# Kernel optimization log

Hardware: AMD Instinct MI355X
Metric: run time of the kernel (lower is better)

## Reference

```python
import jax, jax.numpy as jnp
import numpy as np

B, S, D, H, DFF = 2, 2048, 1024, 16, 4096
DK = D // H
EPS = float(np.finfo(np.float32).eps)  # torch RMSNorm default eps = finfo eps


def rmsnorm(x, g):
    var = jnp.mean(x * x, axis=-1, keepdims=True)
    return x * jax.lax.rsqrt(var + EPS) * g


def rope_cos_sin(seq_len, dim, base=10000.0):
    inv_freq = 1.0 / (base ** (jnp.arange(0, dim, 2, dtype=jnp.float32) / dim))
    t = jnp.arange(seq_len, dtype=jnp.float32)
    freqs = jnp.outer(t, inv_freq)            # [S, dim/2]
    emb = jnp.concatenate([freqs, freqs], -1)  # [S, dim]
    return jnp.cos(emb), jnp.sin(emb)


def rotate_half(x):
    x1, x2 = x[..., : x.shape[-1] // 2], x[..., x.shape[-1] // 2:]
    return jnp.concatenate([-x2, x1], axis=-1)


def setup_inputs() -> dict:
    key = jax.random.key(0)
    ks = jax.random.split(key, 16)
    sc = 0.02
    return {
        "x": jax.random.normal(ks[0], (B, S, D), jnp.float32),
        "wq": jax.random.normal(ks[1], (D, D), jnp.float32) * sc,
        "bq": jnp.zeros((D,), jnp.float32),
        "wk": jax.random.normal(ks[2], (D, D), jnp.float32) * sc,
        "bk": jnp.zeros((D,), jnp.float32),
        "wv": jax.random.normal(ks[3], (D, D), jnp.float32) * sc,
        "bv": jnp.zeros((D,), jnp.float32),
        "wo": jax.random.normal(ks[4], (D, D), jnp.float32) * sc,
        "bo": jnp.zeros((D,), jnp.float32),
        "w1": jax.random.normal(ks[5], (D, DFF), jnp.float32) * sc,
        "b1": jnp.zeros((DFF,), jnp.float32),
        "w2": jax.random.normal(ks[6], (DFF, D), jnp.float32) * sc,
        "b2": jnp.zeros((D,), jnp.float32),
        "g1": jnp.ones((D,), jnp.float32),
        "g2": jnp.ones((D,), jnp.float32),
    }


def reference(x, wq, bq, wk, bk, wv, bv, wo, bo, w1, b1, w2, b2, g1, g2):
    b, s, d = x.shape
    # --- self-attention sublayer (pre-RMSNorm residual) ---
    h = rmsnorm(x, g1)
    q = (h @ wq + bq).reshape(b, s, H, DK).transpose(0, 2, 1, 3)  # [B,H,S,dk]
    k = (h @ wk + bk).reshape(b, s, H, DK).transpose(0, 2, 1, 3)
    v = (h @ wv + bv).reshape(b, s, H, DK).transpose(0, 2, 1, 3)
    cos, sin = rope_cos_sin(s, DK)
    cos = cos[None, None]  # [1,1,S,dk]
    sin = sin[None, None]
    q = q * cos + rotate_half(q) * sin
    k = k * cos + rotate_half(k) * sin
    scores = jnp.einsum("bhqd,bhkd->bhqk", q, k) / jnp.sqrt(jnp.float32(DK))
    p = jax.nn.softmax(scores, axis=-1)
    o = jnp.einsum("bhqk,bhkd->bhqd", p, v)
    o = o.transpose(0, 2, 1, 3).reshape(b, s, d)
    attn_out = o @ wo + bo
    x = x + attn_out
    # --- feed-forward sublayer ---
    h2 = rmsnorm(x, g2)
    ff = jax.nn.relu(h2 @ w1 + b1) @ w2 + b2
    return x + ff
```

## Files before the change

### kernel.cpp

```cpp
#include <hip/hip_runtime.h>
#include <math.h>

typedef unsigned short u16;
typedef __attribute__((ext_vector_type(8))) short bf16x8;
typedef __attribute__((ext_vector_type(4))) float f32x4;
typedef __attribute__((ext_vector_type(4))) unsigned int u32x4;

#define B_ 2
#define S_ 2048
#define D_ 1024
#define H_ 16
#define DK_ 64
#define DFF_ 4096
#define EPS_ 1.1920928955078125e-07f
#define EXP2SC 0.18033688011112042f

__device__ __forceinline__ float bf2f(u16 u) {
  unsigned int v = ((unsigned int)u) << 16;
  return __builtin_bit_cast(float, v);
}
__device__ __forceinline__ u16 f2bf(float f) {
  unsigned int x = __builtin_bit_cast(unsigned int, f);
  x += 0x7fffu + ((x >> 16) & 1u);
  return (u16)(x >> 16);
}

typedef __attribute__((address_space(3))) unsigned int lds_uint;
typedef const __attribute__((address_space(1))) unsigned int glb_uint;
__device__ __forceinline__ void gload16(const void* g, void* l) {
  __builtin_amdgcn_global_load_lds((glb_uint*)g, (lds_uint*)l, 16, 0, 0);
}

__device__ __forceinline__ unsigned int cvtpk(float lo, float hi) {
  unsigned int d;
  asm("v_cvt_pk_bf16_f32 %0, %1, %2" : "=v"(d) : "v"(lo), "v"(hi));
  return d;
}
__device__ __forceinline__ void plswap32(unsigned int& a, unsigned int& b) {
  asm("v_permlane32_swap_b32 %0, %1" : "+v"(a), "+v"(b));
}
__device__ __forceinline__ void plswap16(unsigned int& a, unsigned int& b) {
  asm("v_permlane16_swap_b32 %0, %1" : "+v"(a), "+v"(b));
}

__global__ __launch_bounds__(256) void rope_table(float* __restrict__ cosT,
                                                  float* __restrict__ sinT) {
  int idx = blockIdx.x * 256 + threadIdx.x;
  if (idx >= S_ * 32) return;
  int s = idx >> 5, i = idx & 31;
  double inv = exp(((double)(-2 * i) / (double)DK_) * log(10000.0));
  double ang = (double)s * inv;
  cosT[idx] = (float)cos(ang);
  sinT[idx] = (float)sin(ang);
}

__global__ __launch_bounds__(256) void convertT(const float* __restrict__ src,
                                                u16* __restrict__ dst, int R, int C) {
  __shared__ float t[32][33];
  int c0 = blockIdx.x * 32, r0 = blockIdx.y * 32;
  int tx = threadIdx.x, ty = threadIdx.y;
#pragma unroll
  for (int i = 0; i < 32; i += 8)
    t[ty + i][tx] = src[(size_t)(r0 + ty + i) * C + (c0 + tx)];
  __syncthreads();
#pragma unroll
  for (int i = 0; i < 32; i += 8)
    dst[(size_t)(c0 + ty + i) * R + (r0 + tx)] = f2bf(t[tx][ty + i]);
}

__global__ __launch_bounds__(256) void rmsnorm_k(const float* __restrict__ X,
                                                 const float* __restrict__ g,
                                                 u16* __restrict__ out) {
  const int row = blockIdx.x;
  const float* xr = X + (size_t)row * D_;
  u16* orow = out + (size_t)row * D_;
  const int tid = threadIdx.x;
  float vals[4];
  float s = 0.f;
#pragma unroll
  for (int j = 0; j < 4; j++) {
    float v = xr[tid + j * 256];
    vals[j] = v;
    s += v * v;
  }
#pragma unroll
  for (int off = 32; off > 0; off >>= 1) s += __shfl_down(s, off, 64);
  __shared__ float red[4];
  __shared__ float ssc;
  int lane = tid & 63, wave = tid >> 6;
  if (lane == 0) red[wave] = s;
  __syncthreads();
  if (tid == 0) ssc = 1.0f / sqrtf((red[0] + red[1] + red[2] + red[3]) * (1.0f / D_) + EPS_);
  __syncthreads();
  float sc = ssc;
#pragma unroll
  for (int j = 0; j < 4; j++) {
    int i = tid + j * 256;
    orow[i] = f2bf(vals[j] * sc * g[i]);
  }
}

#define GEMM_KLOOP(APTR, BPTR, KLEN, KLD)                                              \
  for (int k0 = 0; k0 < (KLEN); k0 += 64) {                                            \
    _Pragma("unroll")                                                                  \
    for (int p = 0; p < 2; p++) {                                                      \
      _Pragma("unroll")                                                                \
      for (int c = wave; c < BM / 16; c += 4) {                                        \
        const u16* gp = (APTR) + (size_t)(m0 + c * 16 + lrow) * (KLD) + k0 + p * 32 + lcol; \
        gload16(gp, (char*)As + __builtin_amdgcn_readfirstlane(p * (BM * 64) + c * 1024)); \
      }                                                                                \
      _Pragma("unroll")                                                                \
      for (int c = wave; c < BN / 16; c += 4) {                                        \
        const u16* gp = (BPTR) + (size_t)(n0 + c * 16 + lrow) * (KLD) + k0 + p * 32 + lcol; \
        gload16(gp, (char*)Bs + __builtin_amdgcn_readfirstlane(p * (BN * 64) + c * 1024)); \
      }                                                                                \
    }                                                                                  \
    __syncthreads();                                                                   \
    _Pragma("unroll")                                                                  \
    for (int p = 0; p < 2; p++) {                                                      \
      bf16x8 af[WR], bfv[WC];                                                          \
      _Pragma("unroll")                                                                \
      for (int i = 0; i < WR; i++)                                                     \
        af[i] = *(const bf16x8*)&As[p * (BM * 32) + (wm + i * 16 + l16) * 32 + quad * 8]; \
      _Pragma("unroll")                                                                \
      for (int j = 0; j < WC; j++)                                                     \
        bfv[j] = *(const bf16x8*)&Bs[p * (BN * 32) + (wn + j * 16 + l16) * 32 + quad * 8]; \
      _Pragma("unroll")                                                                \
      for (int i = 0; i < WR; i++)                                                     \
        _Pragma("unroll")                                                              \
        for (int j = 0; j < WC; j++)                                                   \
          acc[i][j] = __builtin_amdgcn_mfma_f32_16x16x32_bf16(af[i], bfv[j], acc[i][j], 0, 0, 0); \
    }                                                                                  \
    __syncthreads();                                                                   \
  }

template <int MODE, int WR, int WC>
__global__ __launch_bounds__(256) void gemm_bt(
    const u16* __restrict__ A, const u16* __restrict__ Bt, const float* __restrict__ bias,
    u16* __restrict__ outB, float* __restrict__ outF, const float* __restrict__ resF,
    int M, int N, int K) {
  constexpr int BM = 2 * WR * 16;
  constexpr int BN = 2 * WC * 16;
  __shared__ u16 As[BM * 64];
  __shared__ u16 Bs[BN * 64];
  const int tid = threadIdx.x;
  const int wave = tid >> 6, lane = tid & 63, quad = lane >> 4, l16 = lane & 15;
  const int wm = (wave >> 1) * (WR * 16), wn = (wave & 1) * (WC * 16);
  const int m0 = blockIdx.y * BM, n0 = blockIdx.x * BN;
  const int lrow = lane >> 2, lcol = (lane & 3) * 8;
  f32x4 acc[WR][WC] = {};
  GEMM_KLOOP(A, Bt, K, K)
#pragma unroll
  for (int i = 0; i < WR; i++)
#pragma unroll
    for (int j = 0; j < WC; j++) {
      int col = n0 + wn + j * 16 + l16;
      float bv = bias[col];
#pragma unroll
      for (int r = 0; r < 4; r++) {
        int row = m0 + wm + i * 16 + quad * 4 + r;
        size_t off = (size_t)row * N + col;
        float v = acc[i][j][r] + bv;
        if constexpr (MODE == 1) v = fmaxf(v, 0.f);
        if constexpr (MODE == 2) outF[off] = v + resF[off];
        else outB[off] = f2bf(v);
      }
    }
}

__global__ __launch_bounds__(256) void gemm_qkv(
    const u16* __restrict__ A, const u16* __restrict__ Bt,
    const float* __restrict__ bq, const float* __restrict__ bk, const float* __restrict__ bv,
    const float* __restrict__ cosT, const float* __restrict__ sinT,
    u16* __restrict__ Qb, u16* __restrict__ Kb, u16* __restrict__ VT, int M, int K) {
  constexpr int WR = 4, WC = 4;
  constexpr int BM = 128, BN = 128;
  __shared__ u16 As[BM * 64];
  __shared__ u16 Bs[BN * 64];
  const int tid = threadIdx.x;
  const int wave = tid >> 6, lane = tid & 63, quad = lane >> 4, l16 = lane & 15;
  const int wm = (wave >> 1) * 64, wn = (wave & 1) * 64;
  const int m0 = blockIdx.y * BM, n0 = blockIdx.x * BN;
  const int lrow = lane >> 2, lcol = (lane & 3) * 8;
  f32x4 acc[WR][WC] = {};
  GEMM_KLOOP(A, Bt, K, K)
  const int g = n0 >> 10;
  if (g < 2) {
    u16* dst = (g == 0) ? Qb : Kb;
    const float* bias = (g == 0) ? bq : bk;
#pragma unroll
    for (int i = 0; i < WR; i++)
#pragma unroll
      for (int jp = 0; jp < 2; jp++) {
        int col0 = n0 + wn + jp * 16 + l16;
        int c0 = col0 & 1023;
        float bv0 = bias[c0], bv1 = bias[c0 + 32];
        int irot = jp * 16 + l16;
        int row0 = m0 + wm + i * 16 + quad * 4;
#pragma unroll
        for (int r = 0; r < 4; r++) {
          int row = row0 + r;
          int s2 = row & 2047;
          float cs = cosT[s2 * 32 + irot];
          float sn = sinT[s2 * 32 + irot];
          float x0 = acc[i][jp][r] + bv0;
          float x1 = acc[i][jp + 2][r] + bv1;
          dst[(size_t)row * D_ + c0]      = f2bf(x0 * cs - x1 * sn);
          dst[(size_t)row * D_ + c0 + 32] = f2bf(x1 * cs + x0 * sn);
        }
      }
  } else {
#pragma unroll
    for (int i = 0; i < WR; i++)
#pragma unroll
      for (int j = 0; j < WC; j++) {
        int col = n0 + wn + j * 16 + l16;
        int c = col & 1023;
        float bvv = bv[c];
        int row0 = m0 + wm + i * 16 + quad * 4;
        int hh = c >> 6, dk = c & 63;
        int b = row0 >> 11, s2 = row0 & 2047;
        ushort4 pv;
        pv.x = f2bf(acc[i][j][0] + bvv);
        pv.y = f2bf(acc[i][j][1] + bvv);
        pv.z = f2bf(acc[i][j][2] + bvv);
        pv.w = f2bf(acc[i][j][3] + bvv);
        *(ushort4*)&VT[(((size_t)(b * H_ + hh)) * DK_ + dk) * S_ + s2] = pv;
      }
  }
}

template <int WR, int WC>
__global__ __launch_bounds__(256) void gemm_splitk(
    const u16* __restrict__ A, const u16* __restrict__ Bt, const float* __restrict__ bias,
    float* outF, int M, int N, int Kslice, int Kld) {
  constexpr int BM = 2 * WR * 16;
  constexpr int BN = 2 * WC * 16;
  __shared__ u16 As[BM * 64];
  __shared__ u16 Bs[BN * 64];
  const int tid = threadIdx.x;
  const int wave = tid >> 6, lane = tid & 63, quad = lane >> 4, l16 = lane & 15;
  const int wm = (wave >> 1) * (WR * 16), wn = (wave & 1) * (WC * 16);
  const int m0 = blockIdx.y * BM, n0 = blockIdx.x * BN;
  const int lrow = lane >> 2, lcol = (lane & 3) * 8;
  const u16* Ao = A + (size_t)blockIdx.z * Kslice;
  const u16* Bo = Bt + (size_t)blockIdx.z * Kslice;
  f32x4 acc[WR][WC] = {};
  GEMM_KLOOP(Ao, Bo, Kslice, Kld)
  const bool addb = (blockIdx.z == 0);
#pragma unroll
  for (int i = 0; i < WR; i++)
#pragma unroll
    for (int j = 0; j < WC; j++) {
      int col = n0 + wn + j * 16 + l16;
      float bv = addb ? bias[col] : 0.f;
#pragma unroll
      for (int r = 0; r < 4; r++) {
        int row = m0 + wm + i * 16 + quad * 4 + r;
        unsafeAtomicAdd(&outF[(size_t)row * N + col], acc[i][j][r] + bv);
      }
    }
}

__device__ __forceinline__ float softmax_pack(f32x4 s0, f32x4 s1, f32x4 s2, f32x4 s3,
                                              bf16x8& pf0, bf16x8& pf1) {
  f32x4 p0, p1, p2, p3;
#pragma unroll
  for (int r = 0; r < 4; r++) {
    p0[r] = exp2f(s0[r] * EXP2SC);
    p1[r] = exp2f(s1[r] * EXP2SC);
    p2[r] = exp2f(s2[r] * EXP2SC);
    p3[r] = exp2f(s3[r] * EXP2SC);
  }
  f32x4 t = (p0 + p1) + (p2 + p3);
  float ls = (t[0] + t[1]) + (t[2] + t[3]);
  unsigned int X0 = cvtpk(p0[0], p0[1]), X1 = cvtpk(p0[2], p0[3]);
  unsigned int Y0 = cvtpk(p1[0], p1[1]), Y1 = cvtpk(p1[2], p1[3]);
  unsigned int Z0 = cvtpk(p2[0], p2[1]), Z1 = cvtpk(p2[2], p2[3]);
  unsigned int W0 = cvtpk(p3[0], p3[1]), W1 = cvtpk(p3[2], p3[3]);
  plswap32(X0, Y0); plswap16(X0, Y0);
  plswap32(X1, Y1); plswap16(X1, Y1);
  plswap32(Z0, W0); plswap16(Z0, W0);
  plswap32(Z1, W1); plswap16(Z1, W1);
  u32x4 lo = {X0, X1, Y0, Y1};
  u32x4 hi = {Z0, Z1, W0, W1};
  pf0 = __builtin_bit_cast(bf16x8, lo);
  pf1 = __builtin_bit_cast(bf16x8, hi);
  return ls;
}

__global__ __launch_bounds__(256, 2) void flash_attn(u16* __restrict__ Q,
                                                     const u16* __restrict__ Kg,
                                                     const u16* __restrict__ VT) {
  const int bh = blockIdx.y;
  const int b = bh >> 4, h = bh & 15;
  const int q0 = blockIdx.x * 128;
  const int tid = threadIdx.x;
  const int wave = tid >> 6, lane = tid & 63, quad = lane >> 4, l16 = lane & 15;
  const size_t base = (size_t)b * S_ * D_ + h * DK_;
  const size_t vbase = (size_t)bh * DK_ * S_;

  __shared__ u16 Ks[2][8192];
  __shared__ u16 Vts[2][8192];

  const int kkey = wave * 32 + (lane >> 3);
  const int kcol = ((lane & 7) ^ (lane >> 3)) * 8;
  const u16* kp0 = Kg + base + (size_t)kkey * D_ + kcol;
  const int vdk0 = wave * 16 + (lane >> 4);
  const int vsel = lane & 15;
  const u16* vp0 = VT + vbase + (size_t)vdk0 * S_;

#define STAGE(BU, KT)                                                                  \
  _Pragma("unroll")                                                                    \
  for (int c = 0; c < 4; c++) {                                                        \
    gload16(kp0 + (size_t)((KT) + c * 8) * D_,                                         \
            (char*)Ks + __builtin_amdgcn_readfirstlane((BU) * 16384 + wave * 4096 + c * 1024)); \
    int vdk = vdk0 + c * 4;                                                            \
    gload16(vp0 + (size_t)(c * 4) * S_ + (KT) + ((vsel ^ (vdk & 7)) * 8),              \
            (char*)Vts + __builtin_amdgcn_readfirstlane((BU) * 16384 + wave * 4096 + c * 1024)); \
  }

  STAGE(0, 0)

  const size_t qoffA = base + (size_t)(q0 + wave * 32 + l16) * D_ + quad * 8;
  const size_t qoffB = qoffA + (size_t)16 * D_;
  bf16x8 qa0 = *(const bf16x8*)(Q + qoffA);
  bf16x8 qa1 = *(const bf16x8*)(Q + qoffA + 32);
  bf16x8 qb0 = *(const bf16x8*)(Q + qoffB);
  bf16x8 qb1 = *(const bf16x8*)(Q + qoffB + 32);

  f32x4 oa[4] = {}, ob[4] = {};
  float lsa = 0.f, lsb = 0.f;
  const int sw = (l16 & 7) << 4;

#define COMPUTE(BU)                                                                    \
  {                                                                                    \
    const char* KsB = (const char*)Ks + (BU) * 16384;                                  \
    const char* VtsB = (const char*)Vts + (BU) * 16384;                                \
    _Pragma("unroll")                                                                  \
    for (int half = 0; half < 2; half++) {                                             \
      f32x4 sa[4] = {}, sb[4] = {};                                                    \
      __builtin_amdgcn_s_setprio(1);                                                   \
      _Pragma("unroll")                                                                \
      for (int nt = 0; nt < 4; nt++) {                                                 \
        const int kr = half * 64 + nt * 16 + l16;                                      \
        const char* krow = KsB + kr * 128;                                             \
        bf16x8 k0 = *(const bf16x8*)(krow + ((quad * 16) ^ sw));                       \
        bf16x8 k1 = *(const bf16x8*)(krow + ((64 + quad * 16) ^ sw));                  \
        sa[nt] = __builtin_amdgcn_mfma_f32_16x16x32_bf16(k0, qa0, sa[nt], 0, 0, 0);    \
        sa[nt] = __builtin_amdgcn_mfma_f32_16x16x32_bf16(k1, qa1, sa[nt], 0, 0, 0);    \
        sb[nt] = __builtin_amdgcn_mfma_f32_16x16x32_bf16(k0, qb0, sb[nt], 0, 0, 0);    \
        sb[nt] = __builtin_amdgcn_mfma_f32_16x16x32_bf16(k1, qb1, sb[nt], 0, 0, 0);    \
      }                                                                                \
      __builtin_amdgcn_s_setprio(0);                                                   \
      bf16x8 pa0, pa1, pb0, pb1;                                                       \
      lsa += softmax_pack(sa[0], sa[1], sa[2], sa[3], pa0, pa1);                       \
      lsb += softmax_pack(sb[0], sb[1], sb[2], sb[3], pb0, pb1);                       \
      __builtin_amdgcn_s_setprio(1);                                                   \
      _Pragma("unroll")                                                                \
      for (int nt = 0; nt < 4; nt++) {                                                 \
        const int vr = nt * 16 + l16;                                                  \
        const char* vrow = VtsB + vr * 256;                                            \
        bf16x8 v0 = *(const bf16x8*)(vrow + ((half * 128 + quad * 16) ^ sw));          \
        bf16x8 v1 = *(const bf16x8*)(vrow + ((half * 128 + 64 + quad * 16) ^ sw));     \
        oa[nt] = __builtin_amdgcn_mfma_f32_16x16x32_bf16(pa0, v0, oa[nt], 0, 0, 0);    \
        oa[nt] = __builtin_amdgcn_mfma_f32_16x16x32_bf16(pa1, v1, oa[nt], 0, 0, 0);    \
        ob[nt] = __builtin_amdgcn_mfma_f32_16x16x32_bf16(pb0, v0, ob[nt], 0, 0, 0);    \
        ob[nt] = __builtin_amdgcn_mfma_f32_16x16x32_bf16(pb1, v1, ob[nt], 0, 0, 0);    \
      }                                                                                \
      __builtin_amdgcn_s_setprio(0);                                                   \
    }                                                                                  \
  }

  for (int kt = 0; kt < S_; kt += 256) {
    __syncthreads();
    STAGE(1, kt + 128)
    COMPUTE(0)
    __syncthreads();
    if (kt + 256 < S_) { STAGE(0, kt + 256) }
    COMPUTE(1)
  }
#undef STAGE
#undef COMPUTE

  lsa += __shfl_xor(lsa, 16, 64);
  lsa += __shfl_xor(lsa, 32, 64);
  lsb += __shfl_xor(lsb, 16, 64);
  lsb += __shfl_xor(lsb, 32, 64);
#pragma unroll
  for (int r = 0; r < 4; r++) {
    float inva = 1.0f / __shfl(lsa, quad * 4 + r, 64);
    float invb = 1.0f / __shfl(lsb, quad * 4 + r, 64);
    const size_t aoff = base + (size_t)(q0 + wave * 32 + quad * 4 + r) * D_;
    const size_t boff = aoff + (size_t)16 * D_;
#pragma unroll
    for (int nt = 0; nt < 4; nt++) {
      Q[aoff + nt * 16 + l16] = f2bf(oa[nt][r] * inva);
      Q[boff + nt * 16 + l16] = f2bf(ob[nt][r] * invb);
    }
  }
}

extern "C" void kernel_launch(void* const* d_in, const int* in_sizes, int n_in,
                              void* d_out, int out_size, void* d_ws, size_t ws_size,
                              hipStream_t stream) {
  const float* x  = (const float*)d_in[0];
  const float* wq = (const float*)d_in[1];
  const float* bq = (const float*)d_in[2];
  const float* wk = (const float*)d_in[3];
  const float* bk = (const float*)d_in[4];
  const float* wv = (const float*)d_in[5];
  const float* bv = (const float*)d_in[6];
  const float* wo = (const float*)d_in[7];
  const float* bo = (const float*)d_in[8];
  const float* w1 = (const float*)d_in[9];
  const float* b1 = (const float*)d_in[10];
  const float* w2 = (const float*)d_in[11];
  const float* b2 = (const float*)d_in[12];
  const float* g1 = (const float*)d_in[13];
  const float* g2 = (const float*)d_in[14];

  char* ws = (char*)d_ws;
  const size_t MB = 1024 * 1024;
  u16* qkvT = (u16*)(ws + 0 * MB);
  u16* woT  = (u16*)(ws + 6 * MB);
  u16* h    = (u16*)(ws + 8 * MB);
  u16* Qb   = (u16*)(ws + 16 * MB);
  u16* Kb   = (u16*)(ws + 24 * MB);
  float* cosT = (float*)(ws + 32 * MB);
  float* sinT = (float*)(ws + 32 * MB + 256 * 1024);
  u16* w2T  = (u16*)(ws + 0 * MB);
  u16* w1T  = (u16*)(ws + 16 * MB);
  u16* f1   = (u16*)(ws + 24 * MB);
  u16* h2   = h;
  u16* Ob   = Qb;
  u16* VT   = (u16*)d_out;
  float* x2 = (float*)d_out;
  const bool bigffn = (ws_size >= 57 * MB);

  const int MS = B_ * S_;
  dim3 tb32(32, 8);
  rope_table<<<(S_ * 32 + 255) / 256, 256, 0, stream>>>(cosT, sinT);
  convertT<<<dim3(32, 32), tb32, 0, stream>>>(wq, qkvT, D_, D_);
  convertT<<<dim3(32, 32), tb32, 0, stream>>>(wk, qkvT + (size_t)D_ * D_, D_, D_);
  convertT<<<dim3(32, 32), tb32, 0, stream>>>(wv, qkvT + 2 * (size_t)D_ * D_, D_, D_);
  convertT<<<dim3(32, 32), tb32, 0, stream>>>(wo, woT, D_, D_);

  rmsnorm_k<<<MS, 256, 0, stream>>>(x, g1, h);
  gemm_qkv<<<dim3(3 * D_ / 128, MS / 128), 256, 0, stream>>>(h, qkvT, bq, bk, bv, cosT, sinT, Qb, Kb, VT, MS, D_);
  flash_attn<<<dim3(S_ / 128, B_ * H_), 256, 0, stream>>>(Qb, Kb, VT);
  gemm_bt<2, 4, 2><<<dim3(D_ / 64, MS / 128), 256, 0, stream>>>(Ob, woT, bo, nullptr, x2, x, MS, D_, D_);

  convertT<<<dim3(DFF_ / 32, D_ / 32), tb32, 0, stream>>>(w1, w1T, D_, DFF_);
  convertT<<<dim3(D_ / 32, DFF_ / 32), tb32, 0, stream>>>(w2, w2T, DFF_, D_);
  rmsnorm_k<<<MS, 256, 0, stream>>>(x2, g2, h2);
  if (bigffn) {
    gemm_bt<1, 4, 4><<<dim3(DFF_ / 128, MS / 128), 256, 0, stream>>>(h2, w1T, b1, f1, nullptr, nullptr, MS, DFF_, D_);
    gemm_splitk<4, 2><<<dim3(D_ / 64, MS / 128, 2), 256, 0, stream>>>(f1, w2T, b2, x2, MS, D_, 2048, DFF_);
  } else {
    for (int i = 0; i < 2; i++) {
      const u16* h2h = h2 + (size_t)i * 2048 * D_;
      float* x2h = x2 + (size_t)i * 2048 * D_;
      gemm_bt<1, 4, 4><<<dim3(DFF_ / 128, 2048 / 128), 256, 0, stream>>>(h2h, w1T, b1, f1, nullptr, nullptr, 2048, DFF_, D_);
      gemm_splitk<4, 2><<<dim3(D_ / 64, 2048 / 128, 2), 256, 0, stream>>>(f1, w2T, b2, x2h, 2048, D_, 2048, DFF_);
    }
  }
  (void)in_sizes; (void)n_in; (void)out_size;
}
```

Measured before the change: 384.3 us.

## Fold softmax scale into Q projection and compute row sums with MFMA

Folds the exp2 softmax scale into the Q projection epilogue, so the attention kernel exponentiates raw scores without a multiply. Row sums of P are now accumulated by MFMA against a ones vector, which removes the VALU reduction and the cross-lane shuffles at the end. All QK products for a tile are computed before any softmax, which gives more independent work to schedule. The risks are higher register pressure, extra bf16 rounding of the scaled Q, and row sums taken from bf16-rounded P values.

```diff
diff --git a/kernel.cpp b/kernel.cpp
--- a/kernel.cpp
+++ b/kernel.cpp
@@ -188,6 +188,7 @@
   if (g < 2) {
     u16* dst = (g == 0) ? Qb : Kb;
     const float* bias = (g == 0) ? bq : bk;
+    const float scq = (g == 0) ? EXP2SC : 1.0f;
 #pragma unroll
     for (int i = 0; i < WR; i++)
 #pragma unroll
@@ -205,8 +206,8 @@
           float sn = sinT[s2 * 32 + irot];
           float x0 = acc[i][jp][r] + bv0;
           float x1 = acc[i][jp + 2][r] + bv1;
-          dst[(size_t)row * D_ + c0]      = f2bf(x0 * cs - x1 * sn);
-          dst[(size_t)row * D_ + c0 + 32] = f2bf(x1 * cs + x0 * sn);
+          dst[(size_t)row * D_ + c0]      = f2bf((x0 * cs - x1 * sn) * scq);
+          dst[(size_t)row * D_ + c0 + 32] = f2bf((x1 * cs + x0 * sn) * scq);
         }
       }
   } else {
@@ -262,18 +263,16 @@
     }
 }
 
-__device__ __forceinline__ float softmax_pack(f32x4 s0, f32x4 s1, f32x4 s2, f32x4 s3,
-                                              bf16x8& pf0, bf16x8& pf1) {
+__device__ __forceinline__ void softmax_pack(f32x4 s0, f32x4 s1, f32x4 s2, f32x4 s3,
+                                             bf16x8& pf0, bf16x8& pf1) {
   f32x4 p0, p1, p2, p3;
 #pragma unroll
   for (int r = 0; r < 4; r++) {
-    p0[r] = exp2f(s0[r] * EXP2SC);
-    p1[r] = exp2f(s1[r] * EXP2SC);
-    p2[r] = exp2f(s2[r] * EXP2SC);
-    p3[r] = exp2f(s3[r] * EXP2SC);
-  }
-  f32x4 t = (p0 + p1) + (p2 + p3);
-  float ls = (t[0] + t[1]) + (t[2] + t[3]);
+    p0[r] = exp2f(s0[r]);
+    p1[r] = exp2f(s1[r]);
+    p2[r] = exp2f(s2[r]);
+    p3[r] = exp2f(s3[r]);
+  }
   unsigned int X0 = cvtpk(p0[0], p0[1]), X1 = cvtpk(p0[2], p0[3]);
   unsigned int Y0 = cvtpk(p1[0], p1[1]), Y1 = cvtpk(p1[2], p1[3]);
   unsigned int Z0 = cvtpk(p2[0], p2[1]), Z1 = cvtpk(p2[2], p2[3]);
@@ -286,7 +285,6 @@
   u32x4 hi = {Z0, Z1, W0, W1};
   pf0 = __builtin_bit_cast(bf16x8, lo);
   pf1 = __builtin_bit_cast(bf16x8, hi);
-  return ls;
 }
 
 __global__ __launch_bounds__(256, 2) void flash_attn(u16* __restrict__ Q,
@@ -330,67 +328,75 @@
   bf16x8 qb1 = *(const bf16x8*)(Q + qoffB + 32);
 
   f32x4 oa[4] = {}, ob[4] = {};
-  float lsa = 0.f, lsb = 0.f;
+  f32x4 lsa_acc = {}, lsb_acc = {};
+  const u32x4 onesu = {0x3F803F80u, 0x3F803F80u, 0x3F803F80u, 0x3F803F80u};
+  const bf16x8 ones = __builtin_bit_cast(bf16x8, onesu);
   const int sw = (l16 & 7) << 4;
 
-#define COMPUTE(BU)                                                                    \
+#define TILE(BU)                                                                       \
   {                                                                                    \
     const char* KsB = (const char*)Ks + (BU) * 16384;                                  \
     const char* VtsB = (const char*)Vts + (BU) * 16384;                                \
+    f32x4 sa[2][4] = {}, sb[2][4] = {};                                                \
+    __builtin_amdgcn_s_setprio(1);                                                     \
     _Pragma("unroll")                                                                  \
     for (int half = 0; half < 2; half++) {                                             \
-      f32x4 sa[4] = {}, sb[4] = {};                                                    \
-      __builtin_amdgcn_s_setprio(1);                                                   \
       _Pragma("unroll")                                                                \
       for (int nt = 0; nt < 4; nt++) {                                                 \
         const int kr = half * 64 + nt * 16 + l16;                                      \
         const char* krow = KsB + kr * 128;                                             \
         bf16x8 k0 = *(const bf16x8*)(krow + ((quad * 16) ^ sw));                       \
         bf16x8 k1 = *(const bf16x8*)(krow + ((64 + quad * 16) ^ sw));                  \
-        sa[nt] = __builtin_amdgcn_mfma_f32_16x16x32_bf16(k0, qa0, sa[nt], 0, 0, 0);    \
-        sa[nt] = __builtin_amdgcn_mfma_f32_16x16x32_bf16(k1, qa1, sa[nt], 0, 0, 0);    \
-        sb[nt] = __builtin_amdgcn_mfma_f32_16x16x32_bf16(k0, qb0, sb[nt], 0, 0, 0);    \
-        sb[nt] = __builtin_amdgcn_mfma_f32_16x16x32_bf16(k1, qb1, sb[nt], 0, 0, 0);    \
+        sa[half][nt] = __builtin_amdgcn_mfma_f32_16x16x32_bf16(k0, qa0, sa[half][nt], 0, 0, 0); \
+        sa[half][nt] = __builtin_amdgcn_mfma_f32_16x16x32_bf16(k1, qa1, sa[half][nt], 0, 0, 0); \
+        sb[half][nt] = __builtin_amdgcn_mfma_f32_16x16x32_bf16(k0, qb0, sb[half][nt], 0, 0, 0); \
+        sb[half][nt] = __builtin_amdgcn_mfma_f32_16x16x32_bf16(k1, qb1, sb[half][nt], 0, 0, 0); \
       }                                                                                \
-      __builtin_amdgcn_s_setprio(0);                                                   \
-      bf16x8 pa0, pa1, pb0, pb1;                                                       \
-      lsa += softmax_pack(sa[0], sa[1], sa[2], sa[3], pa0, pa1);                       \
-      lsb += softmax_pack(sb[0], sb[1], sb[2], sb[3], pb0, pb1);                       \
-      __builtin_amdgcn_s_setprio(1);                                                   \
+    }                                                                                  \
+    __builtin_amdgcn_s_setprio(0);                                                     \
+    bf16x8 pa[2][2], pb[2][2];                                                         \
+    _Pragma("unroll")                                                                  \
+    for (int half = 0; half < 2; half++) {                                             \
+      softmax_pack(sa[half][0], sa[half][1], sa[half][2], sa[half][3], pa[half][0], pa[half][1]); \
+      softmax_pack(sb[half][0], sb[half][1], sb[half][2], sb[half][3], pb[half][0], pb[half][1]); \
+    }                                                                                  \
+    __builtin_amdgcn_s_setprio(1);                                                     \
+    _Pragma("unroll")                                                                  \
+    for (int half = 0; half < 2; half++) {                                             \
+      lsa_acc = __builtin_amdgcn_mfma_f32_16x16x32_bf16(pa[half][0], ones, lsa_acc, 0, 0, 0); \
+      lsa_acc = __builtin_amdgcn_mfma_f32_16x16x32_bf16(pa[half][1], ones, lsa_acc, 0, 0, 0); \
+      lsb_acc = __builtin_amdgcn_mfma_f32_16x16x32_bf16(pb[half][0], ones, lsb_acc, 0, 0, 0); \
+      lsb_acc = __builtin_amdgcn_mfma_f32_16x16x32_bf16(pb[half][1], ones, lsb_acc, 0, 0, 0); \
       _Pragma("unroll")                                                                \
       for (int nt = 0; nt < 4; nt++) {                                                 \
         const int vr = nt * 16 + l16;                                                  \
         const char* vrow = VtsB + vr * 256;                                            \
         bf16x8 v0 = *(const bf16x8*)(vrow + ((half * 128 + quad * 16) ^ sw));          \
         bf16x8 v1 = *(const bf16x8*)(vrow + ((half * 128 + 64 + quad * 16) ^ sw));     \
-        oa[nt] = __builtin_amdgcn_mfma_f32_16x16x32_bf16(pa0, v0, oa[nt], 0, 0, 0);    \
-        oa[nt] = __builtin_amdgcn_mfma_f32_16x16x32_bf16(pa1, v1, oa[nt], 0, 0, 0);    \
-        ob[nt] = __builtin_amdgcn_mfma_f32_16x16x32_bf16(pb0, v0, ob[nt], 0, 0, 0);    \
-        ob[nt] = __builtin_amdgcn_mfma_f32_16x16x32_bf16(pb1, v1, ob[nt], 0, 0, 0);    \
+        oa[nt] = __builtin_amdgcn_mfma_f32_16x16x32_bf16(pa[half][0], v0, oa[nt], 0, 0, 0); \
+        oa[nt] = __builtin_amdgcn_mfma_f32_16x16x32_bf16(pa[half][1], v1, oa[nt], 0, 0, 0); \
+        ob[nt] = __builtin_amdgcn_mfma_f32_16x16x32_bf16(pb[half][0], v0, ob[nt], 0, 0, 0); \
+        ob[nt] = __builtin_amdgcn_mfma_f32_16x16x32_bf16(pb[half][1], v1, ob[nt], 0, 0, 0); \
       }                                                                                \
-      __builtin_amdgcn_s_setprio(0);                                                   \
     }                                                                                  \
+    __builtin_amdgcn_s_setprio(0);                                                     \
   }
 
   for (int kt = 0; kt < S_; kt += 256) {
     __syncthreads();
     STAGE(1, kt + 128)
-    COMPUTE(0)
+    TILE(0)
     __syncthreads();
     if (kt + 256 < S_) { STAGE(0, kt + 256) }
-    COMPUTE(1)
+    TILE(1)
   }
 #undef STAGE
-#undef COMPUTE
-
-  lsa += __shfl_xor(lsa, 16, 64);
-  lsa += __shfl_xor(lsa, 32, 64);
-  lsb += __shfl_xor(lsb, 16, 64);
-  lsb += __shfl_xor(lsb, 32, 64);
+#undef TILE
+
 #pragma unroll
   for (int r = 0; r < 4; r++) {
-    float inva = 1.0f / __shfl(lsa, quad * 4 + r, 64);
-    float invb = 1.0f / __shfl(lsb, quad * 4 + r, 64);
+    float inva = 1.0f / lsa_acc[r];
+    float invb = 1.0f / lsb_acc[r];
     const size_t aoff = base + (size_t)(q0 + wave * 32 + quad * 4 + r) * D_;
     const size_t boff = aoff + (size_t)16 * D_;
 #pragma unroll
```

Measured after the change: 381.6 us. About the same (-0.7%).
